# Kernel optimization log

Measured on AMD Instinct MI355X. Metric: run time of the kernel, lower is better.

## Reference

```python
import jax, jax.numpy as jnp
import numpy as np

N_NEURONS, RANK, N_CONV, LY, LX, BATCH = 8192, 1, 64, 36, 36, 256


def setup_inputs() -> dict:
    key = jax.random.key(0)
    k1, k2, k3, k4 = jax.random.split(key, 4)
    conv = jax.random.normal(k1, (BATCH, N_CONV, LY, LX), dtype=jnp.float32)
    Wc = 0.01 * jax.random.normal(k2, (N_NEURONS, RANK, N_CONV), dtype=jnp.float32)
    Wy = 0.01 * jax.random.normal(k3, (N_NEURONS, RANK, LY), dtype=jnp.float32)
    Wx = 0.01 * jax.random.normal(k4, (N_NEURONS, RANK, LX), dtype=jnp.float32)
    bias = jnp.zeros((N_NEURONS,), dtype=jnp.float32)
    return {"conv": conv, "Wc": Wc, "Wy": Wy, "Wx": Wx, "bias": bias}


def reference(conv, Wc, Wy, Wx, bias):
    # yx_separable, rank == 1 path of Readout.forward:
    #   pred = einsum('nrc,nry,icyx,nrx->in', Wc, Wy, conv, Wx)
    #   pred = elu(pred + bias)
    # Staged contraction: build per-neuron rank-1 spatial filter, contract
    # spatial dims first (small y*x=1296), then channels.
    Wyx = jnp.einsum('nry,nrx->nryx', Wy, Wx)              # [N, R, Ly, Lx]
    s = jnp.einsum('icyx,nryx->inrc', conv, Wyx)           # [B, N, R, C]
    pred = jnp.einsum('inrc,nrc->in', s, Wc)               # [B, N]
    return jax.nn.elu(pred + bias)
```

## Files before the change

### kernel.cpp

```cpp
#include <hip/hip_runtime.h>
#include <hip/hip_bf16.h>

#define NNEUR 8192
#define NCONV 64
#define LYC   36
#define LXC   36
#define BATCH 256
#define KRAW  1296
#define KPAD  1344
#define ASLOT 168
#define MROWS 16384

typedef __attribute__((ext_vector_type(8))) _Float16 half8;
typedef __attribute__((ext_vector_type(4))) float f32x4;

__device__ __forceinline__ void async_copy16(const void* g, void* l) {
  __builtin_amdgcn_global_load_lds(
      (const __attribute__((address_space(1))) void*)g,
      (__attribute__((address_space(3))) void*)l, 16, 0, 0);
}

__global__ __launch_bounds__(256) void conv_cast_kernel(
    const float* __restrict__ conv, _Float16* __restrict__ A) {
  const int slot = blockIdx.x * 256 + threadIdx.x;
  if (slot >= MROWS * ASLOT) return;
  const int row = slot / ASLOT;
  const int j = slot - row * ASLOT;
  half8 h;
  if (j < 162) {
    const float* s = conv + (size_t)row * KRAW + j * 8;
#pragma unroll
    for (int e = 0; e < 8; e++) h[e] = (_Float16)s[e];
  } else {
#pragma unroll
    for (int e = 0; e < 8; e++) h[e] = (_Float16)0.f;
  }
  *(half8*)(A + (size_t)row * KPAD + j * 8) = h;
}

__global__ __launch_bounds__(256) void build_wyx_kernel(
    const float* __restrict__ Wy, const float* __restrict__ Wx,
    _Float16* __restrict__ B) {
  const int slot = blockIdx.x * 256 + threadIdx.x;
  if (slot >= NNEUR * ASLOT) return;
  const int n = slot / ASLOT;
  const int j = slot - n * ASLOT;
  half8 h;
#pragma unroll
  for (int e = 0; e < 8; e++) {
    const int k = j * 8 + e;
    float v = 0.f;
    if (k < KRAW) {
      const int y = k / LXC;
      const int x = k - y * LXC;
      v = Wy[n * LYC + y] * Wx[n * LXC + x] * 256.f;
    }
    h[e] = (_Float16)v;
  }
  *(half8*)(B + (size_t)n * KPAD + j * 8) = h;
}

__global__ __launch_bounds__(256, 3) void gemm_fused_kernel(
    const _Float16* __restrict__ A, const _Float16* __restrict__ B,
    const float* __restrict__ Wc, const float* __restrict__ bias,
    float* __restrict__ out) {
  __shared__ _Float16 As[128 * 64];
  __shared__ _Float16 Bs[128 * 64];

  const int flat = blockIdx.x;
  const int xcd = flat & 7;
  const int local = flat >> 3;
  const int tileN = (xcd * 8 + (local >> 7)) * 128;
  const int tileM = (local & 127) * 128;

  const int t = threadIdx.x;
  const int lane = t & 63;
  const int wave = t >> 6;
  const int wm = wave >> 1, wn = wave & 1;
  const int quad = lane >> 4, col = lane & 15;

  f32x4 acc[4][4] = {};

  const int rbase = t >> 3;
  const int cchunk = ((t & 7) - rbase) & 7;
  const int koff = cchunk * 8;
  const _Float16* gA = A + (size_t)(tileM + rbase) * KPAD + koff;
  const _Float16* gB = B + (size_t)(tileN + rbase) * KPAD + koff;
  _Float16* lA = As + t * 8;
  _Float16* lB = Bs + t * 8;

  for (int kk = 0; kk < KPAD; kk += 64) {
#pragma unroll
    for (int i = 0; i < 4; i++) {
      async_copy16(gA + kk + (size_t)(32 * i) * KPAD, lA + i * 2048);
      async_copy16(gB + kk + (size_t)(32 * i) * KPAD, lB + i * 2048);
    }
    __syncthreads();

#pragma unroll
    for (int s = 0; s < 2; s++) {
      half8 af[4], bfr[4];
#pragma unroll
      for (int ms = 0; ms < 4; ms++) {
        const int r = wm * 64 + ms * 16 + col;
        af[ms] = *(const half8*)(As + r * 64 + (((s << 2) + quad + r) & 7) * 8);
      }
#pragma unroll
      for (int ns = 0; ns < 4; ns++) {
        const int r = wn * 64 + ns * 16 + col;
        bfr[ns] = *(const half8*)(Bs + r * 64 + (((s << 2) + quad + r) & 7) * 8);
      }
#pragma unroll
      for (int ms = 0; ms < 4; ms++)
#pragma unroll
        for (int ns = 0; ns < 4; ns++)
          acc[ms][ns] = __builtin_amdgcn_mfma_f32_16x16x32_f16(
              af[ms], bfr[ns], acc[ms][ns], 0, 0, 0);
    }
    __syncthreads();
  }

  const int i_idx = (tileM >> 6) + wm;
  float red[4];
#pragma unroll
  for (int ns = 0; ns < 4; ns++) {
    const int n_g = tileN + wn * 64 + ns * 16 + col;
    const float* wc = Wc + (size_t)n_g * NCONV;
    float p = 0.f;
#pragma unroll
    for (int ms = 0; ms < 4; ms++) {
      const f32x4 w = *(const f32x4*)(wc + ms * 16 + quad * 4);
      p += acc[ms][ns][0] * w[0] + acc[ms][ns][1] * w[1] +
           acc[ms][ns][2] * w[2] + acc[ms][ns][3] * w[3];
    }
    p += __shfl_xor(p, 16);
    p += __shfl_xor(p, 32);
    red[ns] = p;
  }
  float v = quad == 0 ? red[0] : quad == 1 ? red[1] : quad == 2 ? red[2] : red[3];
  const int n_out = tileN + wn * 64 + quad * 16 + col;
  v = v * 0.00390625f + bias[n_out];
  v = v > 0.f ? v : (__expf(v) - 1.f);
  out[(size_t)i_idx * NNEUR + n_out] = v;
}

extern "C" void kernel_launch(void* const* d_in, const int* in_sizes, int n_in,
                              void* d_out, int out_size, void* d_ws,
                              size_t ws_size, hipStream_t stream) {
  const float* conv = (const float*)d_in[0];
  const float* Wc = (const float*)d_in[1];
  const float* Wy = (const float*)d_in[2];
  const float* Wx = (const float*)d_in[3];
  const float* bias = (const float*)d_in[4];
  float* out = (float*)d_out;

  _Float16* Abuf = (_Float16*)d_ws;
  _Float16* Bbuf = (_Float16*)((char*)d_ws + (size_t)MROWS * KPAD * 2);

  conv_cast_kernel<<<(MROWS * ASLOT + 255) / 256, 256, 0, stream>>>(conv, Abuf);
  build_wyx_kernel<<<(NNEUR * ASLOT + 255) / 256, 256, 0, stream>>>(Wy, Wx, Bbuf);

  gemm_fused_kernel<<<8192, 256, 0, stream>>>(Abuf, Bbuf, Wc, bias, out);
}
```

Measured before the change: 531.9 us.

## Use 256x128 tiles with 32x32 MFMA and pre-tiled swizzled operand layout

Operands are prepacked into per-tile, per-K-iteration contiguous swizzled chunks, so each GEMM block streams linear memory. The two prep kernels are merged into one launch. The GEMM tile grows from 128x128 to 256x128 and switches to 32x32x16 MFMA instructions, which cuts B reloads and LDS reads per FLOP. In exchange LDS use and register pressure rise, the grid is halved to 4096 blocks, and the Wc epilogue reduction is rewritten for the new accumulator layout.

Measured after the change: 481.1 us. 9.5% less time.

```diff
diff --git a/kernel.cpp b/kernel.cpp
--- a/kernel.cpp
+++ b/kernel.cpp
@@ -8,11 +8,19 @@
 #define BATCH 256
 #define KRAW  1296
 #define KPAD  1344
-#define ASLOT 168
+#define KITER 21
 #define MROWS 16384
+#define BM 256
+#define BN 128
+#define BK 64
+#define ACH_PER_IT 2048
+#define BCH_PER_IT 1024
+#define A_TILE_H   (KITER * ACH_PER_IT * 8)
+#define B_TILE_H   (KITER * BCH_PER_IT * 8)
 
 typedef __attribute__((ext_vector_type(8))) _Float16 half8;
 typedef __attribute__((ext_vector_type(4))) float f32x4;
+typedef __attribute__((ext_vector_type(16))) float f32x16;
 
 __device__ __forceinline__ void async_copy16(const void* g, void* l) {
   __builtin_amdgcn_global_load_lds(
@@ -20,128 +28,144 @@
       (__attribute__((address_space(3))) void*)l, 16, 0, 0);
 }
 
-__global__ __launch_bounds__(256) void conv_cast_kernel(
-    const float* __restrict__ conv, _Float16* __restrict__ A) {
-  const int slot = blockIdx.x * 256 + threadIdx.x;
-  if (slot >= MROWS * ASLOT) return;
-  const int row = slot / ASLOT;
-  const int j = slot - row * ASLOT;
+__global__ __launch_bounds__(256) void prep_kernel(
+    const float* __restrict__ conv, const float* __restrict__ Wy,
+    const float* __restrict__ Wx, _Float16* __restrict__ A,
+    _Float16* __restrict__ B) {
+  const int t = threadIdx.x;
+  const int bx = blockIdx.x;
+  const int tile = blockIdx.y;
+  const int slot = t & 7;
   half8 h;
-  if (j < 162) {
-    const float* s = conv + (size_t)row * KRAW + j * 8;
+  if (bx < 168) {
+    const int it = bx >> 3, i = bx & 7;
+    const int r = (t >> 3) + 32 * i;
+    const int c = (slot - r) & 7;
+    const int k0 = it * 64 + c * 8;
+    const int grow = tile * BM + r;
+    if (k0 < KRAW) {
+      const float* s = conv + (size_t)grow * KRAW + k0;
 #pragma unroll
-    for (int e = 0; e < 8; e++) h[e] = (_Float16)s[e];
+      for (int e = 0; e < 8; e++) h[e] = (_Float16)s[e];
+    } else {
+#pragma unroll
+      for (int e = 0; e < 8; e++) h[e] = (_Float16)0.f;
+    }
+    *(half8*)(A + (size_t)tile * A_TILE_H + ((size_t)bx * 256 + t) * 8) = h;
   } else {
+    const int bx4 = bx - 168;
+    const int it = bx4 >> 2, i = bx4 & 3;
+    const int r = (t >> 3) + 32 * i;
+    const int c = (slot - r) & 7;
+    const int k0 = it * 64 + c * 8;
+    const int n = tile * BN + r;
 #pragma unroll
-    for (int e = 0; e < 8; e++) h[e] = (_Float16)0.f;
+    for (int e = 0; e < 8; e++) {
+      const int k = k0 + e;
+      float v = 0.f;
+      if (k < KRAW) {
+        const int y = k / LXC;
+        const int x = k - y * LXC;
+        v = Wy[n * LYC + y] * Wx[n * LXC + x] * 256.f;
+      }
+      h[e] = (_Float16)v;
+    }
+    *(half8*)(B + (size_t)tile * B_TILE_H + ((size_t)bx4 * 256 + t) * 8) = h;
   }
-  *(half8*)(A + (size_t)row * KPAD + j * 8) = h;
-}
-
-__global__ __launch_bounds__(256) void build_wyx_kernel(
-    const float* __restrict__ Wy, const float* __restrict__ Wx,
-    _Float16* __restrict__ B) {
-  const int slot = blockIdx.x * 256 + threadIdx.x;
-  if (slot >= NNEUR * ASLOT) return;
-  const int n = slot / ASLOT;
-  const int j = slot - n * ASLOT;
-  half8 h;
-#pragma unroll
-  for (int e = 0; e < 8; e++) {
-    const int k = j * 8 + e;
-    float v = 0.f;
-    if (k < KRAW) {
-      const int y = k / LXC;
-      const int x = k - y * LXC;
-      v = Wy[n * LYC + y] * Wx[n * LXC + x] * 256.f;
-    }
-    h[e] = (_Float16)v;
-  }
-  *(half8*)(B + (size_t)n * KPAD + j * 8) = h;
 }
 
 __global__ __launch_bounds__(256, 3) void gemm_fused_kernel(
     const _Float16* __restrict__ A, const _Float16* __restrict__ B,
     const float* __restrict__ Wc, const float* __restrict__ bias,
     float* __restrict__ out) {
-  __shared__ _Float16 As[128 * 64];
-  __shared__ _Float16 Bs[128 * 64];
+  __shared__ _Float16 As[BM * BK];
+  __shared__ _Float16 Bs[BN * BK];
 
-  const int flat = blockIdx.x;
-  const int xcd = flat & 7;
-  const int local = flat >> 3;
-  const int tileN = (xcd * 8 + (local >> 7)) * 128;
-  const int tileM = (local & 127) * 128;
+  const int bid = blockIdx.x;
+  const int l = bid >> 3;
+  const int ntile = (bid & 7) * 8 + (l & 7);
+  const int mtile = l >> 3;
+  const int tileN = ntile * BN;
+  const int tileM = mtile * BM;
 
   const int t = threadIdx.x;
   const int lane = t & 63;
   const int wave = t >> 6;
   const int wm = wave >> 1, wn = wave & 1;
-  const int quad = lane >> 4, col = lane & 15;
+  const int r32 = lane & 31, hh = lane >> 5;
 
-  f32x4 acc[4][4] = {};
+  f32x16 acc[4][2] = {};
 
-  const int rbase = t >> 3;
-  const int cchunk = ((t & 7) - rbase) & 7;
-  const int koff = cchunk * 8;
-  const _Float16* gA = A + (size_t)(tileM + rbase) * KPAD + koff;
-  const _Float16* gB = B + (size_t)(tileN + rbase) * KPAD + koff;
+  const _Float16* pA = A + (size_t)mtile * A_TILE_H;
+  const _Float16* pB = B + (size_t)ntile * B_TILE_H;
   _Float16* lA = As + t * 8;
   _Float16* lB = Bs + t * 8;
 
-  for (int kk = 0; kk < KPAD; kk += 64) {
+  for (int it = 0; it < KITER; it++) {
+    const _Float16* sA = pA + (size_t)it * (ACH_PER_IT * 8) + t * 8;
+    const _Float16* sB = pB + (size_t)it * (BCH_PER_IT * 8) + t * 8;
 #pragma unroll
-    for (int i = 0; i < 4; i++) {
-      async_copy16(gA + kk + (size_t)(32 * i) * KPAD, lA + i * 2048);
-      async_copy16(gB + kk + (size_t)(32 * i) * KPAD, lB + i * 2048);
-    }
+    for (int i = 0; i < 8; i++) async_copy16(sA + i * 2048, lA + i * 2048);
+#pragma unroll
+    for (int i = 0; i < 4; i++) async_copy16(sB + i * 2048, lB + i * 2048);
     __syncthreads();
 
 #pragma unroll
-    for (int s = 0; s < 2; s++) {
-      half8 af[4], bfr[4];
+    for (int ks = 0; ks < 4; ks++) {
+      const int cc = 2 * ks + hh;
+      half8 bf[2];
 #pragma unroll
-      for (int ms = 0; ms < 4; ms++) {
-        const int r = wm * 64 + ms * 16 + col;
-        af[ms] = *(const half8*)(As + r * 64 + (((s << 2) + quad + r) & 7) * 8);
+      for (int nb = 0; nb < 2; nb++) {
+        const int r = wn * 64 + nb * 32 + r32;
+        bf[nb] = *(const half8*)(Bs + r * 64 + ((cc + r) & 7) * 8);
       }
 #pragma unroll
-      for (int ns = 0; ns < 4; ns++) {
-        const int r = wn * 64 + ns * 16 + col;
-        bfr[ns] = *(const half8*)(Bs + r * 64 + (((s << 2) + quad + r) & 7) * 8);
+      for (int mb = 0; mb < 4; mb++) {
+        const int r = wm * 128 + mb * 32 + r32;
+        const half8 af = *(const half8*)(As + r * 64 + ((cc + r) & 7) * 8);
+#pragma unroll
+        for (int nb = 0; nb < 2; nb++)
+          acc[mb][nb] = __builtin_amdgcn_mfma_f32_32x32x16_f16(
+              af, bf[nb], acc[mb][nb], 0, 0, 0);
       }
-#pragma unroll
-      for (int ms = 0; ms < 4; ms++)
-#pragma unroll
-        for (int ns = 0; ns < 4; ns++)
-          acc[ms][ns] = __builtin_amdgcn_mfma_f32_16x16x32_f16(
-              af[ms], bfr[ns], acc[ms][ns], 0, 0, 0);
     }
     __syncthreads();
   }
 
-  const int i_idx = (tileM >> 6) + wm;
-  float red[4];
+  const int ibase = mtile * 4 + wm * 2;
+  float v[2][2];
 #pragma unroll
-  for (int ns = 0; ns < 4; ns++) {
-    const int n_g = tileN + wn * 64 + ns * 16 + col;
+  for (int nb = 0; nb < 2; nb++) {
+    const int n_g = tileN + wn * 64 + nb * 32 + r32;
     const float* wc = Wc + (size_t)n_g * NCONV;
-    float p = 0.f;
+    f32x4 w[2][4];
 #pragma unroll
-    for (int ms = 0; ms < 4; ms++) {
-      const f32x4 w = *(const f32x4*)(wc + ms * 16 + quad * 4);
-      p += acc[ms][ns][0] * w[0] + acc[ms][ns][1] * w[1] +
-           acc[ms][ns][2] * w[2] + acc[ms][ns][3] * w[3];
+    for (int hf = 0; hf < 2; hf++)
+#pragma unroll
+      for (int g = 0; g < 4; g++)
+        w[hf][g] = *(const f32x4*)(wc + hf * 32 + hh * 4 + g * 8);
+#pragma unroll
+    for (int img = 0; img < 2; img++) {
+      float p = 0.f;
+#pragma unroll
+      for (int hf = 0; hf < 2; hf++)
+#pragma unroll
+        for (int g = 0; g < 4; g++)
+#pragma unroll
+          for (int q = 0; q < 4; q++)
+            p += acc[img * 2 + hf][nb][g * 4 + q] * w[hf][g][q];
+      p += __shfl_xor(p, 32);
+      v[img][nb] = p;
     }
-    p += __shfl_xor(p, 16);
-    p += __shfl_xor(p, 32);
-    red[ns] = p;
   }
-  float v = quad == 0 ? red[0] : quad == 1 ? red[1] : quad == 2 ? red[2] : red[3];
-  const int n_out = tileN + wn * 64 + quad * 16 + col;
-  v = v * 0.00390625f + bias[n_out];
-  v = v > 0.f ? v : (__expf(v) - 1.f);
-  out[(size_t)i_idx * NNEUR + n_out] = v;
+  const int img = ibase + hh;
+#pragma unroll
+  for (int nb = 0; nb < 2; nb++) {
+    const int n_out = tileN + wn * 64 + nb * 32 + r32;
+    float z = v[hh][nb] * 0.00390625f + bias[n_out];
+    z = z > 0.f ? z : (__expf(z) - 1.f);
+    out[(size_t)img * NNEUR + n_out] = z;
+  }
 }
 
 extern "C" void kernel_launch(void* const* d_in, const int* in_sizes, int n_in,
@@ -157,8 +181,6 @@
   _Float16* Abuf = (_Float16*)d_ws;
   _Float16* Bbuf = (_Float16*)((char*)d_ws + (size_t)MROWS * KPAD * 2);
 
-  conv_cast_kernel<<<(MROWS * ASLOT + 255) / 256, 256, 0, stream>>>(conv, Abuf);
-  build_wyx_kernel<<<(NNEUR * ASLOT + 255) / 256, 256, 0, stream>>>(Wy, Wx, Bbuf);
-
-  gemm_fused_kernel<<<8192, 256, 0, stream>>>(Abuf, Bbuf, Wc, bias, out);
+  prep_kernel<<<dim3(252, 64), 256, 0, stream>>>(conv, Wy, Wx, Abuf, Bbuf);
+  gemm_fused_kernel<<<4096, 256, 0, stream>>>(Abuf, Bbuf, Wc, bias, out);
 }
```
